# Performance work log

Hardware: AMD Instinct MI355X
Metric: run time of the kernel (lower is better)

Reference implementation:

```python
import jax, jax.numpy as jnp
import numpy as np

# EKV constants from Config
VT = 0.025
N_FACTOR = 1.5
VD = 0.5
ALPHA = 2e-06
BASE_TIA = 500000.0

KERNEL = 3
STRIDE = 1
PAD = 1


def _unfold(x, k, stride, pad):
    # torch.nn.functional.unfold: (N, C, H, W) -> (N, C*k*k, L), patch dims ordered (c, kh, kw)
    N, C, H, W = x.shape
    xp = jnp.pad(x, ((0, 0), (0, 0), (pad, pad), (pad, pad)))
    Ho = (H + 2 * pad - k) // stride + 1
    Wo = (W + 2 * pad - k) // stride + 1
    patches = []
    for i in range(k):
        for j in range(k):
            patches.append(xp[:, :, i:i + stride * Ho:stride, j:j + stride * Wo:stride])
    # (k*k, N, C, Ho, Wo) -> (N, C, k*k, Ho*Wo) -> (N, C*k*k, L)
    p = jnp.stack(patches, axis=2)  # (N, C, k*k, Ho, Wo)
    return p.reshape(N, C * k * k, Ho * Wo), Ho, Wo


def setup_inputs() -> dict:
    key = jax.random.key(0)
    k1, k2 = jax.random.split(key)
    x = jax.random.normal(k1, (4, 64, 32, 32), dtype=jnp.float32)
    # theta ~ Normal(2.5, 0.5), shape (out_channels, in_channels, k, k)
    theta = 2.5 + 0.5 * jax.random.normal(k2, (64, 64, 3, 3), dtype=jnp.float32)
    return {"x": x, "theta": theta}


def reference(x, theta):
    N, C, H, W = x.shape
    O = theta.shape[0]
    fan_in = C * KERNEL * KERNEL
    tia_gain = BASE_TIA / (fan_in ** 0.5)
    phi = 2 * N_FACTOR * VT

    x_unf, Ho, Wo = _unfold(x, KERNEL, STRIDE, PAD)      # (N, C*k*k, L)
    x_in = x_unf[:, None, :, :]                           # (N, 1, CKK, L)
    w_th = theta.reshape(1, O, -1, 1)                     # (1, O, CKK, 1)

    v_diff = x_in - w_th                                  # (N, O, CKK, L)
    f_term = jnp.square(jax.nn.softplus(v_diff / phi))
    r_term = jnp.square(jax.nn.softplus((v_diff - VD) / phi))
    i_syn = ALPHA * (f_term - r_term)
    out_current = jnp.sum(i_syn, axis=2)                  # (N, O, L)
    out_voltage = out_current * tia_gain
    return out_voltage.reshape(N, O, Ho, Wo)
```

## Files before the change

### kernel.cpp

```cpp
#include <hip/hip_runtime.h>
#include <math.h>

#define HH 32
#define WW 32
#define CIN 64
#define NO 64
#define NCK 576
#define X_ELEMS 262144

#define WS_W    0
#define WS_TAU  36864
#define WS_END  37504

__device__ __forceinline__ float fexp2(float x) {
#if __has_builtin(__builtin_amdgcn_exp2f)
    return __builtin_amdgcn_exp2f(x);
#else
    return exp2f(x);
#endif
}
__device__ __forceinline__ float flog2(float x) {
#if __has_builtin(__builtin_amdgcn_logf)
    return __builtin_amdgcn_logf(x);
#else
    return log2f(x);
#endif
}

__global__ __launch_bounds__(256) void prep_kernel(const float* __restrict__ theta,
                                                   float* __restrict__ ws) {
    constexpr float SZ = 19.235933878519512f;
    const int b = blockIdx.x, t = threadIdx.x;
    if (b < 144) {
        int i = b * 256 + t;
        int o = i & 63, ck = i >> 6;
        float th = theta[o * NCK + ck];
        ws[WS_W + i] = -SZ * th;
        float mn = th;
#pragma unroll
        for (int s = 32; s > 0; s >>= 1)
            mn = fminf(mn, __shfl_xor(mn, s, 64));
        if (o == 0) ws[WS_TAU + ck] = SZ * mn - 8.0f;
    } else {
        if (t < 64) ws[WS_TAU + NCK + t] = 1e30f;
    }
}

__global__ __launch_bounds__(256) void warm_kernel(const float* __restrict__ x,
                                                   float* __restrict__ ws) {
    const int gid = (int)blockIdx.x * 256 + (int)threadIdx.x;
    float acc = 0.f;
    const float4* w4 = (const float4*)ws;
    for (int i = gid; i < WS_END / 4; i += 128 * 256) acc += w4[i].x + w4[i].w;
    const float4* x4 = (const float4*)x;
    for (int i = gid; i < X_ELEMS / 4; i += 128 * 256) acc += x4[i].x + x4[i].w;
    if (acc == 1234.56789f) ws[WS_END] = acc;
}

__global__ __launch_bounds__(128) void ekv_kernel(
        const float* __restrict__ x, const float* __restrict__ ws,
        float* __restrict__ out) {
    constexpr float SZ = 19.235933878519512f;
    constexpr float C2 = 1.2726342e-3f;
    constexpr float OS = 0.020018875579925058f;

    __shared__ float part[64];

    const int t    = threadIdx.x;
    const int lane = t & 63;
    const int wv   = __builtin_amdgcn_readfirstlane(t >> 6);
    const int pix  = (int)blockIdx.x;
    const int n  = pix >> 10;
    const int ho = (pix >> 5) & 31;
    const int wo = pix & 31;
    const int c0 = wv * 32;

    int l = lane;
    int c_off = l / 9; if (c_off > 6) c_off = 6;
    int k = l - 9 * c_off; if (k > 8) k = 8;
    int di = k / 3, dj = k - 3 * (k / 3);
    int h = ho + di - 1, w_ = wo + dj - 1;
    bool sval = (h >= 0) && (h < HH) && (w_ >= 0) && (w_ < WW);
    int hc = min(max(h, 0), HH - 1), wc = min(max(w_, 0), WW - 1);
    float msc = ((l < 63) && sval) ? SZ : 0.0f;

    int gidx = n * (CIN * HH * WW) + (c0 + c_off) * 1024 + hc * WW + wc;
    const float* tw  = ws + WS_TAU + c0 * 9;
    const float* wsW = ws + WS_W;

    float accF = 0.f, accR = 0.f;

    float xv = x[min(gidx, X_ELEMS - 1)];
    float tv = tw[l];

    for (int cb = 0; cb < 32; cb += 7) {
        int cc = 32 - cb; if (cc > 7) cc = 7;
        int gidx2 = gidx + 7 * 1024;
        const float* tw2 = tw + 63;
        float xvn = xv, tvn = tv;
        if (cb + 7 < 32) { xvn = x[min(gidx2, X_ELEMS - 1)]; tvn = tw2[l]; }

        float xs = xv * msc;
        unsigned long long act = __ballot(xs >= tv);
        act &= (1ull << (cc * 9)) - 1ull;

        const int cb9 = (c0 + cb) * 9;
        while (act) {
            unsigned long long a = act;
            int i0 = (int)__builtin_ctzll(a);             a &= a - 1;
            bool h1 = a != 0;
            int i1 = a ? (int)__builtin_ctzll(a) : 0;     a &= a - 1;
            bool h2 = a != 0;
            int i2 = a ? (int)__builtin_ctzll(a) : 0;     a &= a - 1;
            bool h3 = a != 0;
            int i3 = a ? (int)__builtin_ctzll(a) : 0;     a &= a - 1;
            act = a;
            float W0 = wsW[((cb9 + i0) << 6) + lane];
            float W1 = wsW[((cb9 + i1) << 6) + lane];
            float W2 = wsW[((cb9 + i2) << 6) + lane];
            float W3 = wsW[((cb9 + i3) << 6) + lane];

#define EKV_BODY(II, WV, EN)                                               \
            {                                                              \
                int xb = __builtin_amdgcn_readlane(                        \
                             __builtin_bit_cast(int, xs), (II));           \
                float sx = __builtin_bit_cast(float, xb);                  \
                float z  = (EN) ? (WV) + sx : -200.0f;   \
                float e  = fexp2(z);                                       \
                float f  = flog2(1.0f + e);                                \
                float r  = flog2(fmaf(C2, e, 1.0f));                       \
                accF = fmaf(f, f, accF);                                   \
                accR = fmaf(r, r, accR);                                   \
            }
            EKV_BODY(i0, W0, true)
            EKV_BODY(i1, W1, h1)
            EKV_BODY(i2, W2, h2)
            EKV_BODY(i3, W3, h3)
#undef EKV_BODY
        }
        gidx = gidx2; tw = tw2; xv = xvn; tv = tvn;
    }

    float p = accF - accR;
    if (wv == 1) part[lane] = p;
    __syncthreads();
    if (wv == 0)
        out[((n * NO + lane) * HH + ho) * WW + wo] = (p + part[lane]) * OS;
}

extern "C" void kernel_launch(void* const* d_in, const int* in_sizes, int n_in,
                              void* d_out, int out_size, void* d_ws, size_t ws_size,
                              hipStream_t stream) {
    const float* x     = (const float*)d_in[0];
    const float* theta = (const float*)d_in[1];
    float* out = (float*)d_out;
    float* ws  = (float*)d_ws;

    prep_kernel<<<145, 256, 0, stream>>>(theta, ws);
    warm_kernel<<<128, 256, 0, stream>>>(x, ws);
    ekv_kernel<<<4096, 128, 0, stream>>>(x, ws, out);
}
```

Measured before the change: 79.33 us.

## Stage input halo tile in LDS and process four output pixels per block

Each 512-thread block now loads a zero-padded 64-channel 3x6 halo tile of x into shared memory, and eight waves compute four adjacent output pixels from it instead of reading x from global memory per pixel. The zero padding removes the per-lane boundary mask, and the x prefetch is dropped from the warm-up kernel. This is meant to cut redundant global loads of overlapping 3x3 windows. In exchange it adds a tile load and barrier at block start, and larger blocks may reduce scheduling flexibility.

```diff
diff --git a/kernel.cpp b/kernel.cpp
--- a/kernel.cpp
+++ b/kernel.cpp
@@ -11,6 +11,9 @@
 #define WS_W    0
 #define WS_TAU  36864
 #define WS_END  37504
+
+#define TC 68
+#define TILE_N (TC * 18)
 
 __device__ __forceinline__ float fexp2(float x) {
 #if __has_builtin(__builtin_amdgcn_exp2f)
@@ -46,61 +49,74 @@
     }
 }
 
-__global__ __launch_bounds__(256) void warm_kernel(const float* __restrict__ x,
-                                                   float* __restrict__ ws) {
+__global__ __launch_bounds__(256) void warm_kernel(float* __restrict__ ws) {
     const int gid = (int)blockIdx.x * 256 + (int)threadIdx.x;
     float acc = 0.f;
     const float4* w4 = (const float4*)ws;
-    for (int i = gid; i < WS_END / 4; i += 128 * 256) acc += w4[i].x + w4[i].w;
-    const float4* x4 = (const float4*)x;
-    for (int i = gid; i < X_ELEMS / 4; i += 128 * 256) acc += x4[i].x + x4[i].w;
+    for (int i = gid; i < WS_END / 4; i += 64 * 256) acc += w4[i].x + w4[i].w;
     if (acc == 1234.56789f) ws[WS_END] = acc;
 }
 
-__global__ __launch_bounds__(128) void ekv_kernel(
+__global__ __launch_bounds__(512) void ekv_kernel(
         const float* __restrict__ x, const float* __restrict__ ws,
         float* __restrict__ out) {
     constexpr float SZ = 19.235933878519512f;
     constexpr float C2 = 1.2726342e-3f;
     constexpr float OS = 0.020018875579925058f;
 
-    __shared__ float part[64];
+    __shared__ float xt[TILE_N];
+    __shared__ float part[4][64];
 
-    const int t    = threadIdx.x;
+    const int t   = threadIdx.x;
+    const int grp = (int)blockIdx.x;
+    const int n   = grp >> 8;
+    const int ho  = (grp >> 3) & 31;
+    const int wg  = (grp & 7) << 2;
+
+#pragma unroll
+    for (int pass = 0; pass < 3; ++pass) {
+        int idx = pass * 512 + t;
+        if (idx < TILE_N) {
+            int c  = idx / 18, rem = idx - 18 * c;
+            int hh = rem / 6,  ww2 = rem - 6 * hh;
+            int h = ho - 1 + hh, w = wg - 1 + ww2;
+            float v = 0.f;
+            if (c < CIN && h >= 0 && h < HH && w >= 0 && w < WW)
+                v = x[((n * CIN + c) * HH + h) * WW + w];
+            xt[idx] = v;
+        }
+    }
+    __syncthreads();
+
     const int lane = t & 63;
     const int wv   = __builtin_amdgcn_readfirstlane(t >> 6);
-    const int pix  = (int)blockIdx.x;
-    const int n  = pix >> 10;
-    const int ho = (pix >> 5) & 31;
-    const int wo = pix & 31;
-    const int c0 = wv * 32;
+    const int px   = wv >> 1;
+    const int half = wv & 1;
+    const int c0   = half * 32;
+    const int wo   = wg + px;
 
     int l = lane;
     int c_off = l / 9; if (c_off > 6) c_off = 6;
     int k = l - 9 * c_off; if (k > 8) k = 8;
     int di = k / 3, dj = k - 3 * (k / 3);
-    int h = ho + di - 1, w_ = wo + dj - 1;
-    bool sval = (h >= 0) && (h < HH) && (w_ >= 0) && (w_ < WW);
-    int hc = min(max(h, 0), HH - 1), wc = min(max(w_, 0), WW - 1);
-    float msc = ((l < 63) && sval) ? SZ : 0.0f;
+    int loff = (c0 + c_off) * 18 + di * 6 + px + dj;
 
-    int gidx = n * (CIN * HH * WW) + (c0 + c_off) * 1024 + hc * WW + wc;
     const float* tw  = ws + WS_TAU + c0 * 9;
     const float* wsW = ws + WS_W;
 
     float accF = 0.f, accR = 0.f;
 
-    float xv = x[min(gidx, X_ELEMS - 1)];
+    float xv = xt[loff];
     float tv = tw[l];
 
     for (int cb = 0; cb < 32; cb += 7) {
         int cc = 32 - cb; if (cc > 7) cc = 7;
-        int gidx2 = gidx + 7 * 1024;
+        int loff2 = loff + 7 * 18;
         const float* tw2 = tw + 63;
         float xvn = xv, tvn = tv;
-        if (cb + 7 < 32) { xvn = x[min(gidx2, X_ELEMS - 1)]; tvn = tw2[l]; }
+        if (cb + 7 < 32) { xvn = xt[loff2]; tvn = tw2[l]; }
 
-        float xs = xv * msc;
+        float xs = xv * SZ;
         unsigned long long act = __ballot(xs >= tv);
         act &= (1ull << (cc * 9)) - 1ull;
 
@@ -138,14 +154,14 @@
             EKV_BODY(i3, W3, h3)
 #undef EKV_BODY
         }
-        gidx = gidx2; tw = tw2; xv = xvn; tv = tvn;
+        loff = loff2; tw = tw2; xv = xvn; tv = tvn;
     }
 
     float p = accF - accR;
-    if (wv == 1) part[lane] = p;
+    if (half == 1) part[px][lane] = p;
     __syncthreads();
-    if (wv == 0)
-        out[((n * NO + lane) * HH + ho) * WW + wo] = (p + part[lane]) * OS;
+    if (half == 0)
+        out[((n * NO + lane) * HH + ho) * WW + wo] = (p + part[px][lane]) * OS;
 }
 
 extern "C" void kernel_launch(void* const* d_in, const int* in_sizes, int n_in,
@@ -157,6 +173,6 @@
     float* ws  = (float*)d_ws;
 
     prep_kernel<<<145, 256, 0, stream>>>(theta, ws);
-    warm_kernel<<<128, 256, 0, stream>>>(x, ws);
-    ekv_kernel<<<4096, 128, 0, stream>>>(x, ws, out);
+    warm_kernel<<<64, 256, 0, stream>>>(ws);
+    ekv_kernel<<<1024, 512, 0, stream>>>(x, ws, out);
 }
```

Result: no change. 78.02 us (-1.7%).

## Split active-tap compaction into a build kernel and stream compacted lists in EKV kernel

Applied to the files above, without the earlier changes.

A new build kernel runs the threshold test per pixel-half and writes the active (index, scaled x) pairs into per-wave compacted lists in workspace, padded to multiples of four. The EKV kernel then reads these lists as int4/float4 and evaluates the softplus terms without any ballot or ctz bookkeeping in the inner loop. The cache-warming kernel is removed and blocks are widened to 512 threads. In exchange it adds an extra global write and read of the lists (up to 296 entries per wave), plus one more kernel boundary.

```diff
diff --git a/kernel.cpp b/kernel.cpp
--- a/kernel.cpp
+++ b/kernel.cpp
@@ -7,10 +7,14 @@
 #define NO 64
 #define NCK 576
 #define X_ELEMS 262144
+#define NP2 8192
+#define STRIDE_E 296
 
 #define WS_W    0
 #define WS_TAU  36864
-#define WS_END  37504
+#define WS_N    37504
+#define WS_LC   45696
+#define WS_LX   (WS_LC + NP2 * STRIDE_E)
 
 __device__ __forceinline__ float fexp2(float x) {
 #if __has_builtin(__builtin_amdgcn_exp2f)
@@ -46,34 +50,18 @@
     }
 }
 
-__global__ __launch_bounds__(256) void warm_kernel(const float* __restrict__ x,
-                                                   float* __restrict__ ws) {
-    const int gid = (int)blockIdx.x * 256 + (int)threadIdx.x;
-    float acc = 0.f;
-    const float4* w4 = (const float4*)ws;
-    for (int i = gid; i < WS_END / 4; i += 128 * 256) acc += w4[i].x + w4[i].w;
-    const float4* x4 = (const float4*)x;
-    for (int i = gid; i < X_ELEMS / 4; i += 128 * 256) acc += x4[i].x + x4[i].w;
-    if (acc == 1234.56789f) ws[WS_END] = acc;
-}
-
-__global__ __launch_bounds__(128) void ekv_kernel(
-        const float* __restrict__ x, const float* __restrict__ ws,
-        float* __restrict__ out) {
+__global__ __launch_bounds__(512) void build_kernel(const float* __restrict__ x,
+                                                    float* __restrict__ ws) {
     constexpr float SZ = 19.235933878519512f;
-    constexpr float C2 = 1.2726342e-3f;
-    constexpr float OS = 0.020018875579925058f;
-
-    __shared__ float part[64];
-
     const int t    = threadIdx.x;
     const int lane = t & 63;
     const int wv   = __builtin_amdgcn_readfirstlane(t >> 6);
-    const int pix  = (int)blockIdx.x;
+    const int p2   = (int)blockIdx.x * 8 + wv;
+    const int pix  = p2 >> 1, half = p2 & 1;
     const int n  = pix >> 10;
     const int ho = (pix >> 5) & 31;
     const int wo = pix & 31;
-    const int c0 = wv * 32;
+    const int c0 = half * 32;
 
     int l = lane;
     int c_off = l / 9; if (c_off > 6) c_off = 6;
@@ -85,10 +73,11 @@
     float msc = ((l < 63) && sval) ? SZ : 0.0f;
 
     int gidx = n * (CIN * HH * WW) + (c0 + c_off) * 1024 + hc * WW + wc;
-    const float* tw  = ws + WS_TAU + c0 * 9;
-    const float* wsW = ws + WS_W;
+    const float* tw = ws + WS_TAU + c0 * 9;
 
-    float accF = 0.f, accR = 0.f;
+    int*   listC = (int*)ws + WS_LC + p2 * STRIDE_E;
+    float* listX = ws + WS_LX + p2 * STRIDE_E;
+    int cnt = 0;
 
     float xv = x[min(gidx, X_ELEMS - 1)];
     float tv = tw[l];
@@ -101,51 +90,82 @@
         if (cb + 7 < 32) { xvn = x[min(gidx2, X_ELEMS - 1)]; tvn = tw2[l]; }
 
         float xs = xv * msc;
-        unsigned long long act = __ballot(xs >= tv);
-        act &= (1ull << (cc * 9)) - 1ull;
-
-        const int cb9 = (c0 + cb) * 9;
-        while (act) {
-            unsigned long long a = act;
-            int i0 = (int)__builtin_ctzll(a);             a &= a - 1;
-            bool h1 = a != 0;
-            int i1 = a ? (int)__builtin_ctzll(a) : 0;     a &= a - 1;
-            bool h2 = a != 0;
-            int i2 = a ? (int)__builtin_ctzll(a) : 0;     a &= a - 1;
-            bool h3 = a != 0;
-            int i3 = a ? (int)__builtin_ctzll(a) : 0;     a &= a - 1;
-            act = a;
-            float W0 = wsW[((cb9 + i0) << 6) + lane];
-            float W1 = wsW[((cb9 + i1) << 6) + lane];
-            float W2 = wsW[((cb9 + i2) << 6) + lane];
-            float W3 = wsW[((cb9 + i3) << 6) + lane];
-
-#define EKV_BODY(II, WV, EN)                                               \
-            {                                                              \
-                int xb = __builtin_amdgcn_readlane(                        \
-                             __builtin_bit_cast(int, xs), (II));           \
-                float sx = __builtin_bit_cast(float, xb);                  \
-                float z  = (EN) ? (WV) + sx : -200.0f;   \
-                float e  = fexp2(z);                                       \
-                float f  = flog2(1.0f + e);                                \
-                float r  = flog2(fmaf(C2, e, 1.0f));                       \
-                accF = fmaf(f, f, accF);                                   \
-                accR = fmaf(r, r, accR);                                   \
-            }
-            EKV_BODY(i0, W0, true)
-            EKV_BODY(i1, W1, h1)
-            EKV_BODY(i2, W2, h2)
-            EKV_BODY(i3, W3, h3)
-#undef EKV_BODY
+        bool a = (xs >= tv) && (l < cc * 9);
+        unsigned long long act = __ballot(a);
+        unsigned lo32 = (unsigned)act, hi32 = (unsigned)(act >> 32);
+        int idx = __builtin_amdgcn_mbcnt_hi(hi32,
+                      __builtin_amdgcn_mbcnt_lo(lo32, 0));
+        if (a) {
+            listC[cnt + idx] = (c0 + cb) * 9 + l;
+            listX[cnt + idx] = xs;
         }
+        cnt += __popcll(act);
         gidx = gidx2; tw = tw2; xv = xvn; tv = tvn;
     }
+    int padn = (-cnt) & 3;
+    if (lane < padn) { listC[cnt + lane] = 0; listX[cnt + lane] = -100000.0f; }
+    cnt += padn;
+    if (lane == 0) ((int*)ws)[WS_N + p2] = cnt >> 2;
+}
+
+__global__ __launch_bounds__(512) void ekv_kernel(
+        const float* __restrict__ ws, float* __restrict__ out) {
+    constexpr float C2 = 1.2726342e-3f;
+    constexpr float OS = 0.020018875579925058f;
+
+    __shared__ float part[4][64];
+
+    const int t    = threadIdx.x;
+    const int lane = t & 63;
+    const int wv   = __builtin_amdgcn_readfirstlane(t >> 6);
+    const int p2   = (int)blockIdx.x * 8 + wv;
+    const int pix  = p2 >> 1, half = p2 & 1;
+    const int px   = wv >> 1;
+    const int n  = pix >> 10;
+    const int ho = (pix >> 5) & 31;
+    const int wo = pix & 31;
+
+    const int rounds = ((const int*)ws)[WS_N + p2];
+    const int4*   LC = (const int4*)((const int*)ws + WS_LC + p2 * STRIDE_E);
+    const float4* LX = (const float4*)(ws + WS_LX + p2 * STRIDE_E);
+    const float* wsW = ws + WS_W;
+
+    float accF = 0.f, accR = 0.f;
+
+#define EKV_BODY(SX, WV)                                                   \
+    {                                                                      \
+        float z  = (WV) + (SX);                        \
+        float e  = fexp2(z);                                               \
+        float f  = flog2(1.0f + e);                                        \
+        float rr = flog2(fmaf(C2, e, 1.0f));                               \
+        accF = fmaf(f, f, accF);                                           \
+        accR = fmaf(rr, rr, accR);                                         \
+    }
+
+    if (rounds > 0) {
+        int4   cq = LC[0];
+        float4 xq = LX[0];
+        for (int r = 0; r < rounds; ++r) {
+            int4 cqn = cq; float4 xqn = xq;
+            if (r + 1 < rounds) { cqn = LC[r + 1]; xqn = LX[r + 1]; }
+            float W0 = wsW[(cq.x << 6) + lane];
+            float W1 = wsW[(cq.y << 6) + lane];
+            float W2 = wsW[(cq.z << 6) + lane];
+            float W3 = wsW[(cq.w << 6) + lane];
+            EKV_BODY(xq.x, W0)
+            EKV_BODY(xq.y, W1)
+            EKV_BODY(xq.z, W2)
+            EKV_BODY(xq.w, W3)
+            cq = cqn; xq = xqn;
+        }
+    }
+#undef EKV_BODY
 
     float p = accF - accR;
-    if (wv == 1) part[lane] = p;
+    if (half == 1) part[px][lane] = p;
     __syncthreads();
-    if (wv == 0)
-        out[((n * NO + lane) * HH + ho) * WW + wo] = (p + part[lane]) * OS;
+    if (half == 0)
+        out[((n * NO + lane) * HH + ho) * WW + wo] = (p + part[px][lane]) * OS;
 }
 
 extern "C" void kernel_launch(void* const* d_in, const int* in_sizes, int n_in,
@@ -156,7 +176,7 @@
     float* out = (float*)d_out;
     float* ws  = (float*)d_ws;
 
-    prep_kernel<<<145, 256, 0, stream>>>(theta, ws);
-    warm_kernel<<<128, 256, 0, stream>>>(x, ws);
-    ekv_kernel<<<4096, 128, 0, stream>>>(x, ws, out);
+    prep_kernel <<<145, 256, 0, stream>>>(theta, ws);
+    build_kernel<<<1024, 512, 0, stream>>>(x, ws);
+    ekv_kernel  <<<1024, 512, 0, stream>>>(ws, out);
 }
```

Measured after the change: 78.22 us. No clear change (-1.4%).
